# Kernel optimization log

Hardware: AMD Instinct MI355X
Metric: run time of the kernel (lower is better)

## Reference

```python
import jax, jax.numpy as jnp
import numpy as np

N = 100000   # nodes
E = 1600000  # edges
H = 256      # hidden_channels
C_IN = 1
C_OUT = 6
B = 64       # graphs in batch


def setup_inputs() -> dict:
    key = jax.random.key(0)
    ks = jax.random.split(key, 14)
    x = jax.random.normal(ks[0], (N, C_IN), jnp.float32)
    edge_index = jax.random.randint(ks[1], (2, E), 0, N, dtype=jnp.int64)
    batch = jnp.sort(jax.random.randint(ks[2], (N,), 0, B, dtype=jnp.int64))
    svm_pred = jax.random.uniform(ks[3], (B,), jnp.float32)

    def w(k, shape, fan_in):
        return jax.random.normal(k, shape, jnp.float32) * (1.0 / np.sqrt(fan_in))

    return {
        "x": x, "edge_index": edge_index, "batch": batch, "svm_pred": svm_pred,
        "W1": w(ks[4], (C_IN, H), C_IN),  "b1": jnp.zeros((H,), jnp.float32),
        "W2": w(ks[5], (H, H), H),        "b2": jnp.zeros((H,), jnp.float32),
        "W3": w(ks[6], (H, H), H),        "b3": jnp.zeros((H,), jnp.float32),
        "Wf1": w(ks[7], (H + 1, 128), H + 1), "bf1": jnp.zeros((128,), jnp.float32),
        "Wf2": w(ks[8], (128, C_OUT), 128),   "bf2": jnp.zeros((C_OUT,), jnp.float32),
    }


def reference(x, edge_index, batch, svm_pred,
              W1, b1, W2, b2, W3, b3, Wf1, bf1, Wf2, bf2):
    # --- GCN normalization (PyG GCNConv default: add self-loops, sym norm) ---
    loops = jnp.arange(N, dtype=edge_index.dtype)
    src = jnp.concatenate([edge_index[0], loops])  # [E+N]
    dst = jnp.concatenate([edge_index[1], loops])  # [E+N]
    deg = jax.ops.segment_sum(jnp.ones_like(dst, dtype=x.dtype), dst, num_segments=N)
    dinv = deg ** -0.5  # deg >= 1 due to self-loops
    norm = dinv[src] * dinv[dst]  # [E+N]

    def gcn(h, W, b):
        hw = h @ W                                   # [N, H]
        msg = hw[src] * norm[:, None]                # gather + scale
        return jax.ops.segment_sum(msg, dst, num_segments=N) + b

    # Dropout is identity in eval mode.
    h = jax.nn.relu(gcn(x, W1, b1))
    h = jax.nn.relu(gcn(h, W2, b2))
    h = jax.nn.relu(gcn(h, W3, b3))

    # global_mean_pool over graph ids
    sums = jax.ops.segment_sum(h, batch, num_segments=B)            # [B, H]
    cnts = jax.ops.segment_sum(jnp.ones((N,), h.dtype), batch, num_segments=B)
    pooled = sums / jnp.maximum(cnts, 1.0)[:, None]

    feat = jnp.concatenate([pooled, svm_pred.reshape(-1, 1).astype(h.dtype)], axis=1)
    out = jax.nn.relu(feat @ Wf1 + bf1) @ Wf2 + bf2                 # [B, 6]
    return out
```

## Files before the change

kernel.cpp:

```cpp
#include <hip/hip_runtime.h>
#include <math.h>

#define N_NODES 100000
#define N_EDGES 1600000
#define HDIM    256
#define NGRAPH  64

#define SCAN_BLK 1024
#define SCAN_NB  ((N_NODES + SCAN_BLK - 1) / SCAN_BLK)

#define FB 64

typedef __attribute__((ext_vector_type(8))) short bf16x8;
typedef __attribute__((ext_vector_type(4))) float f32x4;
typedef __attribute__((ext_vector_type(8))) unsigned short u16x8;

__device__ __forceinline__ ushort f2b(float f) {
    union { float f; unsigned u; } x; x.f = f;
    unsigned u = x.u;
    unsigned r = u + 0x7fffu + ((u >> 16) & 1u);
    return (ushort)(r >> 16);
}
__device__ __forceinline__ float b2f(ushort h) {
    union { unsigned u; float f; } x; x.u = ((unsigned)h) << 16;
    return x.f;
}

__global__ void k_count(const int* __restrict__ ei, int* __restrict__ cnt,
                        int* __restrict__ slot) {
    int t = blockIdx.x * blockDim.x + threadIdx.x;
    int e0 = t * 8;
    if (e0 >= N_EDGES) return;
    int d[8];
#pragma unroll
    for (int j = 0; j < 8; ++j) d[j] = ei[N_EDGES + e0 + j];
    int s[8];
#pragma unroll
    for (int j = 0; j < 8; ++j) s[j] = atomicAdd(&cnt[d[j]], 1);
#pragma unroll
    for (int j = 0; j < 8; ++j) slot[e0 + j] = s[j];
}

__global__ __launch_bounds__(1024) void k_scan1(const int* __restrict__ cnt,
                                                int* __restrict__ rowptr,
                                                int* __restrict__ bsum) {
    __shared__ int lds[SCAN_BLK];
    int t = threadIdx.x;
    int i = blockIdx.x * SCAN_BLK + t;
    int v = (i < N_NODES) ? cnt[i] : 0;
    lds[t] = v;
    __syncthreads();
    for (int off = 1; off < SCAN_BLK; off <<= 1) {
        int u = (t >= off) ? lds[t - off] : 0;
        __syncthreads();
        lds[t] += u;
        __syncthreads();
    }
    if (i < N_NODES) rowptr[i] = lds[t] - v;
    if (t == SCAN_BLK - 1) bsum[blockIdx.x] = lds[t];
}

__global__ __launch_bounds__(128) void k_scan2(int* __restrict__ bsum) {
    __shared__ int lds[128];
    int t = threadIdx.x;
    int v = (t < SCAN_NB) ? bsum[t] : 0;
    lds[t] = v;
    __syncthreads();
    for (int off = 1; off < 128; off <<= 1) {
        int u = (t >= off) ? lds[t - off] : 0;
        __syncthreads();
        lds[t] += u;
        __syncthreads();
    }
    if (t < SCAN_NB) bsum[t] = lds[t] - v;
}

__global__ void k_dinv_fix(const int* __restrict__ cnt, const float* __restrict__ x,
                           const int* __restrict__ bsum,
                           float* __restrict__ dinv, float* __restrict__ xd,
                           int* __restrict__ rowptr) {
    int i = blockIdx.x * blockDim.x + threadIdx.x;
    if (i < N_NODES) {
        rowptr[i] += bsum[i >> 10];
        float d = (float)(cnt[i] + 1);
        float dv = 1.0f / sqrtf(d);
        dinv[i] = dv;
        xd[i] = x[i] * dv;
        if (i == 0) rowptr[N_NODES] = N_EDGES;
    }
}

__global__ void k_fill(const int* __restrict__ ei, const int* __restrict__ rowptr,
                       const int* __restrict__ slot, int* __restrict__ colv) {
    int t = blockIdx.x * blockDim.x + threadIdx.x;
    int e0 = t * 4;
    if (e0 >= N_EDGES) return;
    int d[4], sl[4], sr[4];
#pragma unroll
    for (int j = 0; j < 4; ++j) {
        d[j] = ei[N_EDGES + e0 + j];
        sl[j] = slot[e0 + j];
        sr[j] = ei[e0 + j];
    }
    int rp[4];
#pragma unroll
    for (int j = 0; j < 4; ++j) rp[j] = rowptr[d[j]];
#pragma unroll
    for (int j = 0; j < 4; ++j) colv[rp[j] + sl[j]] = sr[j];
}

__global__ __launch_bounds__(256) void k_s(const int* __restrict__ rowptr,
                                           const int* __restrict__ colv,
                                           const float* __restrict__ xd,
                                           const float* __restrict__ dinv,
                                           float2* __restrict__ sd) {
    int wid = threadIdx.x >> 6, lane = threadIdx.x & 63;
    int node = blockIdx.x * 4 + wid;
    if (node >= N_NODES) return;
    int s = rowptr[node], e = rowptr[node + 1];
    float acc = 0.f;
    for (int idx = s + lane; idx < e; idx += 64) acc += xd[colv[idx]];
#pragma unroll
    for (int off = 32; off; off >>= 1) acc += __shfl_xor(acc, off);
    if (lane == 0) {
        float dv = dinv[node];
        sd[node] = make_float2(dv * (acc + xd[node]), dv);
    }
}

__global__ __launch_bounds__(256) void k_aggM(const int* __restrict__ rowptr,
                                              const int* __restrict__ colv,
                                              const float2* __restrict__ sd,
                                              const float* __restrict__ W1,
                                              const float* __restrict__ b1,
                                              ushort* __restrict__ M) {
    int wid = threadIdx.x >> 6, lane = threadIdx.x & 63;
    int node = blockIdx.x * 4 + wid;
    if (node >= N_NODES) return;
    int c4 = lane * 4;
    float4 w = *(const float4*)&W1[c4];
    float4 b = *(const float4*)&b1[c4];
    float2 self = sd[node];
    float a0 = self.y * fmaxf(fmaf(self.x, w.x, b.x), 0.f);
    float a1 = self.y * fmaxf(fmaf(self.x, w.y, b.y), 0.f);
    float a2 = self.y * fmaxf(fmaf(self.x, w.z, b.z), 0.f);
    float a3 = self.y * fmaxf(fmaf(self.x, w.w, b.w), 0.f);
    int s = rowptr[node], e = rowptr[node + 1];
    for (int base = s; base < e; base += 64) {
        int idx = base + lane;
        float2 p = make_float2(0.f, 0.f);
        if (idx < e) p = sd[colv[idx]];
        int rem = min(64, e - base);
        int k = 0;
        for (; k + 4 <= rem; k += 4) {
            float ps0 = __shfl(p.x, k),     pd0 = __shfl(p.y, k);
            float ps1 = __shfl(p.x, k + 1), pd1 = __shfl(p.y, k + 1);
            float ps2 = __shfl(p.x, k + 2), pd2 = __shfl(p.y, k + 2);
            float ps3 = __shfl(p.x, k + 3), pd3 = __shfl(p.y, k + 3);
            a0 += pd0 * fmaxf(fmaf(ps0, w.x, b.x), 0.f)
                + pd1 * fmaxf(fmaf(ps1, w.x, b.x), 0.f)
                + pd2 * fmaxf(fmaf(ps2, w.x, b.x), 0.f)
                + pd3 * fmaxf(fmaf(ps3, w.x, b.x), 0.f);
            a1 += pd0 * fmaxf(fmaf(ps0, w.y, b.y), 0.f)
                + pd1 * fmaxf(fmaf(ps1, w.y, b.y), 0.f)
                + pd2 * fmaxf(fmaf(ps2, w.y, b.y), 0.f)
                + pd3 * fmaxf(fmaf(ps3, w.y, b.y), 0.f);
            a2 += pd0 * fmaxf(fmaf(ps0, w.z, b.z), 0.f)
                + pd1 * fmaxf(fmaf(ps1, w.z, b.z), 0.f)
                + pd2 * fmaxf(fmaf(ps2, w.z, b.z), 0.f)
                + pd3 * fmaxf(fmaf(ps3, w.z, b.z), 0.f);
            a3 += pd0 * fmaxf(fmaf(ps0, w.w, b.w), 0.f)
                + pd1 * fmaxf(fmaf(ps1, w.w, b.w), 0.f)
                + pd2 * fmaxf(fmaf(ps2, w.w, b.w), 0.f)
                + pd3 * fmaxf(fmaf(ps3, w.w, b.w), 0.f);
        }
        for (; k < rem; ++k) {
            float ps = __shfl(p.x, k);
            float pd = __shfl(p.y, k);
            a0 += pd * fmaxf(fmaf(ps, w.x, b.x), 0.f);
            a1 += pd * fmaxf(fmaf(ps, w.y, b.y), 0.f);
            a2 += pd * fmaxf(fmaf(ps, w.z, b.z), 0.f);
            a3 += pd * fmaxf(fmaf(ps, w.w, b.w), 0.f);
        }
    }
    float dvi = self.y;
    ushort4 o;
    o.x = f2b(a0 * dvi);
    o.y = f2b(a1 * dvi);
    o.z = f2b(a2 * dvi);
    o.w = f2b(a3 * dvi);
    *(ushort4*)&M[(size_t)node * HDIM + c4] = o;
}

__global__ __launch_bounds__(256) void k_packW2(const float* __restrict__ Wa,
                                                ushort* __restrict__ Wpa,
                                                const float* __restrict__ Wb,
                                                ushort* __restrict__ Wpb) {
    int bid = blockIdx.x;
    const float* W = (bid < 32) ? Wa : Wb;
    ushort* Wp = (bid < 32) ? Wpa : Wpb;
    int t = (bid & 31) * 256 + threadIdx.x;
    int lane = t & 63;
    int nt = (t >> 6) & 15;
    int k0 = t >> 10;
    int col = nt * 16 + (lane & 15);
    int kb = k0 * 32 + (lane >> 4) * 8;
    ushort o[8];
#pragma unroll
    for (int j = 0; j < 8; ++j) o[j] = f2b(W[(size_t)(kb + j) * HDIM + col]);
    *(ushort4*)&Wp[(size_t)t * 8 + 0] = make_ushort4(o[0], o[1], o[2], o[3]);
    *(ushort4*)&Wp[(size_t)t * 8 + 4] = make_ushort4(o[4], o[5], o[6], o[7]);
}

__global__ __launch_bounds__(256) void k_g23(
    const ushort* __restrict__ M,
    const ushort* __restrict__ Wp2, const float* __restrict__ b2,
    const ushort* __restrict__ Wp3, const float* __restrict__ dinv,
    ushort* __restrict__ C) {
    __shared__ __align__(16) ushort lds[FB * 256];
    char* ldsb = (char*)lds;
    int tid = threadIdx.x;
    int wave = tid >> 6, lane = tid & 63;
    int l = wave * 16 + (lane & 15);
    int node = blockIdx.x * FB + l;
    int kgrp = lane >> 4;
    bool ok = node < N_NODES;
    unsigned swz = ((unsigned)(l & 7)) << 4;
    unsigned rowb = (unsigned)l * 512;

    f32x4 acc[16];
#pragma unroll
    for (int nt = 0; nt < 16; ++nt) acc[nt] = (f32x4){0.f, 0.f, 0.f, 0.f};
    const ushort* ap = M + (size_t)(ok ? node : 0) * HDIM + kgrp * 8;
#pragma unroll 1
    for (int k0 = 0; k0 < 8; ++k0) {
        bf16x8 bf = *(const bf16x8*)(ap + k0 * 32);
        if (!ok) bf = (bf16x8){0, 0, 0, 0, 0, 0, 0, 0};
        const ushort* wp = Wp2 + ((size_t)k0 * 1024 + lane) * 8;
#pragma unroll
        for (int nt = 0; nt < 16; ++nt) {
            bf16x8 a = *(const bf16x8*)(wp + (size_t)nt * 512);
            acc[nt] = __builtin_amdgcn_mfma_f32_16x16x32_bf16(a, bf, acc[nt], 0, 0, 0);
        }
    }

#pragma unroll
    for (int nt = 0; nt < 16; ++nt) {
        int f = nt * 16 + kgrp * 4;
        float4 bv = *(const float4*)&b2[f];
        uint2 pk;
        pk.x = (unsigned)f2b(fmaxf(acc[nt][0] + bv.x, 0.f)) |
               ((unsigned)f2b(fmaxf(acc[nt][1] + bv.y, 0.f)) << 16);
        pk.y = (unsigned)f2b(fmaxf(acc[nt][2] + bv.z, 0.f)) |
               ((unsigned)f2b(fmaxf(acc[nt][3] + bv.w, 0.f)) << 16);
        *(uint2*)(ldsb + rowb + (((unsigned)(f * 2)) ^ swz)) = pk;
    }
    __syncthreads();

#pragma unroll
    for (int nt = 0; nt < 16; ++nt) acc[nt] = (f32x4){0.f, 0.f, 0.f, 0.f};
#pragma unroll 1
    for (int k0 = 0; k0 < 8; ++k0) {
        bf16x8 bf = *(const bf16x8*)(ldsb + rowb + (((unsigned)(16 * kgrp + 64 * k0)) ^ swz));
        const ushort* wp = Wp3 + ((size_t)k0 * 1024 + lane) * 8;
#pragma unroll
        for (int nt = 0; nt < 16; ++nt) {
            bf16x8 a = *(const bf16x8*)(wp + (size_t)nt * 512);
            acc[nt] = __builtin_amdgcn_mfma_f32_16x16x32_bf16(a, bf, acc[nt], 0, 0, 0);
        }
    }
    if (ok) {
        float dv = dinv[node];
        size_t base = (size_t)node * HDIM + kgrp * 4;
#pragma unroll
        for (int nt = 0; nt < 16; ++nt) {
            ushort4 o;
            o.x = f2b(acc[nt][0] * dv);
            o.y = f2b(acc[nt][1] * dv);
            o.z = f2b(acc[nt][2] * dv);
            o.w = f2b(acc[nt][3] * dv);
            *(ushort4*)&C[base + nt * 16] = o;
        }
    }
}

__global__ __launch_bounds__(256) void k_agg(const ushort* __restrict__ g,
                                             const int* __restrict__ rowptr,
                                             const int* __restrict__ colv,
                                             const float* __restrict__ dinv,
                                             const float* __restrict__ bias,
                                             ushort* __restrict__ hout) {
    int wid = threadIdx.x >> 6, lane = threadIdx.x & 63;
    int node = blockIdx.x * 4 + wid;
    if (node >= N_NODES) return;
    int half = lane >> 5;
    int l32 = lane & 31;
    int c8 = l32 * 8;
    float acc[8];
    if (half == 0) {
        u16x8 v = *(const u16x8*)&g[(size_t)node * HDIM + c8];
#pragma unroll
        for (int j = 0; j < 8; ++j) acc[j] = b2f(v[j]);
    } else {
#pragma unroll
        for (int j = 0; j < 8; ++j) acc[j] = 0.f;
    }
    int s = rowptr[node], e = rowptr[node + 1];
    int i = s;
    for (; i + 8 <= e; i += 8) {
        int base = i + half * 4;
        int n0 = colv[base + 0];
        int n1 = colv[base + 1];
        int n2 = colv[base + 2];
        int n3 = colv[base + 3];
        u16x8 v0 = *(const u16x8*)&g[(size_t)n0 * HDIM + c8];
        u16x8 v1 = *(const u16x8*)&g[(size_t)n1 * HDIM + c8];
        u16x8 v2 = *(const u16x8*)&g[(size_t)n2 * HDIM + c8];
        u16x8 v3 = *(const u16x8*)&g[(size_t)n3 * HDIM + c8];
#pragma unroll
        for (int j = 0; j < 8; ++j)
            acc[j] += (b2f(v0[j]) + b2f(v1[j])) + (b2f(v2[j]) + b2f(v3[j]));
    }
    if (i + 4 <= e) {
        int base = i + half * 2;
        int n0 = colv[base + 0];
        int n1 = colv[base + 1];
        u16x8 v0 = *(const u16x8*)&g[(size_t)n0 * HDIM + c8];
        u16x8 v1 = *(const u16x8*)&g[(size_t)n1 * HDIM + c8];
#pragma unroll
        for (int j = 0; j < 8; ++j) acc[j] += b2f(v0[j]) + b2f(v1[j]);
        i += 4;
    }
    if (i + 2 <= e) {
        int n = colv[i + half];
        u16x8 v = *(const u16x8*)&g[(size_t)n * HDIM + c8];
#pragma unroll
        for (int j = 0; j < 8; ++j) acc[j] += b2f(v[j]);
        i += 2;
    }
    if (i < e && half == 0) {
        int n = colv[i];
        u16x8 v = *(const u16x8*)&g[(size_t)n * HDIM + c8];
#pragma unroll
        for (int j = 0; j < 8; ++j) acc[j] += b2f(v[j]);
    }
#pragma unroll
    for (int j = 0; j < 8; ++j) acc[j] += __shfl_xor(acc[j], 32);
    if (half == 0) {
        float dv = dinv[node];
        float4 bl = *(const float4*)&bias[c8];
        float4 bh = *(const float4*)&bias[c8 + 4];
        float bj[8] = {bl.x, bl.y, bl.z, bl.w, bh.x, bh.y, bh.z, bh.w};
        u16x8 ov;
#pragma unroll
        for (int j = 0; j < 8; ++j)
            ov[j] = f2b(fmaxf(fmaf(acc[j], dv, bj[j]), 0.f));
        *(u16x8*)&hout[(size_t)node * HDIM + c8] = ov;
    }
}

__global__ __launch_bounds__(128) void k_bounds(const int* __restrict__ batch,
                                                int* __restrict__ startb,
                                                float* __restrict__ pooled) {
    int t = threadIdx.x;
    if (t <= NGRAPH) {
        int lo = 0, hi = N_NODES;
        while (lo < hi) {
            int mid = (lo + hi) >> 1;
            if (batch[mid] < t) lo = mid + 1; else hi = mid;
        }
        startb[t] = lo;
    }
    for (int i = t; i < NGRAPH * HDIM; i += 128) pooled[i] = 0.f;
}

__global__ __launch_bounds__(256) void k_pool(const ushort* __restrict__ h,
                                              const int* __restrict__ startb,
                                              float* __restrict__ pooled) {
    int b = blockIdx.x >> 3, c = blockIdx.x & 7;
    int s0 = startb[b], e0 = startb[b + 1];
    int len = e0 - s0;
    if (len <= 0) return;
    int per = (len + 7) >> 3;
    int is = s0 + c * per;
    int ie = min(is + per, e0);
    if (is >= ie) return;
    int j = threadIdx.x;
    float sum = 0.f;
    for (int n = is; n < ie; ++n) sum += b2f(h[(size_t)n * HDIM + j]);
    atomicAdd(&pooled[b * HDIM + j], sum);
}

__global__ __launch_bounds__(128) void k_mlp(const float* __restrict__ pooled,
                                             const int* __restrict__ startb,
                                             const float* __restrict__ svm,
                                             const float* __restrict__ Wf1,
                                             const float* __restrict__ bf1,
                                             const float* __restrict__ Wf2,
                                             const float* __restrict__ bf2,
                                             float* __restrict__ out) {
    __shared__ float fl[257];
    __shared__ float hl[128];
    int b = blockIdx.x;
    int j = threadIdx.x;
    float cntb = fmaxf((float)(startb[b + 1] - startb[b]), 1.0f);
    for (int k = j; k < 256; k += 128) fl[k] = pooled[b * HDIM + k] / cntb;
    if (j == 0) fl[256] = svm[b];
    __syncthreads();
    float acc = bf1[j];
    for (int k = 0; k < 257; ++k) acc = fmaf(fl[k], Wf1[k * 128 + j], acc);
    hl[j] = fmaxf(acc, 0.f);
    __syncthreads();
    if (j < 6) {
        float o = bf2[j];
        for (int k = 0; k < 128; ++k) o = fmaf(hl[k], Wf2[k * 6 + j], o);
        out[b * 6 + j] = o;
    }
}

static inline size_t al256(size_t x) { return (x + 255) & ~(size_t)255; }

extern "C" void kernel_launch(void* const* d_in, const int* in_sizes, int n_in,
                              void* d_out, int out_size, void* d_ws, size_t ws_size,
                              hipStream_t stream) {
    const float* x    = (const float*)d_in[0];
    const int*   ei   = (const int*)d_in[1];
    const int*   batch= (const int*)d_in[2];
    const float* svm  = (const float*)d_in[3];
    const float* W1   = (const float*)d_in[4];
    const float* b1   = (const float*)d_in[5];
    const float* W2   = (const float*)d_in[6];
    const float* b2   = (const float*)d_in[7];
    const float* W3   = (const float*)d_in[8];
    const float* b3   = (const float*)d_in[9];
    const float* Wf1  = (const float*)d_in[10];
    const float* bf1  = (const float*)d_in[11];
    const float* Wf2  = (const float*)d_in[12];
    const float* bf2  = (const float*)d_in[13];
    float* out = (float*)d_out;

    char* w = (char*)d_ws;
    int*    cnt    = (int*)w;    w += al256((size_t)N_NODES * 4);
    int*    rowptr = (int*)w;    w += al256((size_t)(N_NODES + 1) * 4);
    int*    slot   = (int*)w;    w += al256((size_t)N_EDGES * 4);
    int*    colv   = (int*)w;    w += al256((size_t)N_EDGES * 4);
    float*  dinv   = (float*)w;  w += al256((size_t)N_NODES * 4);
    float*  xd     = (float*)w;  w += al256((size_t)N_NODES * 4);
    float2* sd     = (float2*)w; w += al256((size_t)N_NODES * 8);
    int*    startb = (int*)w;    w += al256(65 * 4);
    int*    bsum   = (int*)w;    w += al256((size_t)SCAN_NB * 4);
    float*  pooled = (float*)w;  w += al256((size_t)NGRAPH * HDIM * 4);
    ushort* Wp2    = (ushort*)w; w += al256((size_t)8 * 16 * 64 * 8 * 2);
    ushort* Wp3    = (ushort*)w; w += al256((size_t)8 * 16 * 64 * 8 * 2);
    ushort* bigA   = (ushort*)w; w += al256((size_t)N_NODES * HDIM * 2);
    ushort* bigB   = (ushort*)w; w += al256((size_t)N_NODES * HDIM * 2);

    const int nblkN = (N_NODES + 255) / 256;
    const int nblkW = (N_NODES + 3) / 4;
    const int nblkF = (N_NODES + FB - 1) / FB;

    hipMemsetAsync(cnt, 0, (size_t)N_NODES * 4, stream);
    k_count<<<(N_EDGES / 8 + 255) / 256, 256, 0, stream>>>(ei, cnt, slot);
    k_scan1<<<SCAN_NB, SCAN_BLK, 0, stream>>>(cnt, rowptr, bsum);
    k_scan2<<<1, 128, 0, stream>>>(bsum);
    k_dinv_fix<<<nblkN, 256, 0, stream>>>(cnt, x, bsum, dinv, xd, rowptr);
    k_fill<<<(N_EDGES / 4 + 255) / 256, 256, 0, stream>>>(ei, rowptr, slot, colv);

    k_packW2<<<64, 256, 0, stream>>>(W2, Wp2, W3, Wp3);

    k_s<<<nblkW, 256, 0, stream>>>(rowptr, colv, xd, dinv, sd);

    k_aggM<<<nblkW, 256, 0, stream>>>(rowptr, colv, sd, W1, b1, bigA);

    k_g23<<<nblkF, 256, 0, stream>>>(bigA, Wp2, b2, Wp3, dinv, bigB);

    k_agg<<<nblkW, 256, 0, stream>>>(bigB, rowptr, colv, dinv, b3, bigA);

    k_bounds<<<1, 128, 0, stream>>>(batch, startb, pooled);
    k_pool<<<NGRAPH * 8, 256, 0, stream>>>(bigA, startb, pooled);
    k_mlp<<<NGRAPH, 128, 0, stream>>>(pooled, startb, svm, Wf1, bf1, Wf2, bf2, out);
}
```

Baseline: 466.7 us.

## Fuse final GCN aggregation with mean pooling and widen edge-per-thread work

```diff
diff --git a/kernel.cpp b/kernel.cpp
--- a/kernel.cpp
+++ b/kernel.cpp
@@ -29,16 +29,16 @@
 __global__ void k_count(const int* __restrict__ ei, int* __restrict__ cnt,
                         int* __restrict__ slot) {
     int t = blockIdx.x * blockDim.x + threadIdx.x;
-    int e0 = t * 8;
+    int e0 = t * 16;
     if (e0 >= N_EDGES) return;
-    int d[8];
-#pragma unroll
-    for (int j = 0; j < 8; ++j) d[j] = ei[N_EDGES + e0 + j];
-    int s[8];
-#pragma unroll
-    for (int j = 0; j < 8; ++j) s[j] = atomicAdd(&cnt[d[j]], 1);
-#pragma unroll
-    for (int j = 0; j < 8; ++j) slot[e0 + j] = s[j];
+    int d[16];
+#pragma unroll
+    for (int j = 0; j < 16; ++j) d[j] = ei[N_EDGES + e0 + j];
+    int s[16];
+#pragma unroll
+    for (int j = 0; j < 16; ++j) s[j] = atomicAdd(&cnt[d[j]], 1);
+#pragma unroll
+    for (int j = 0; j < 16; ++j) slot[e0 + j] = s[j];
 }
 
 __global__ __launch_bounds__(1024) void k_scan1(const int* __restrict__ cnt,
@@ -93,20 +93,20 @@
 __global__ void k_fill(const int* __restrict__ ei, const int* __restrict__ rowptr,
                        const int* __restrict__ slot, int* __restrict__ colv) {
     int t = blockIdx.x * blockDim.x + threadIdx.x;
-    int e0 = t * 4;
+    int e0 = t * 8;
     if (e0 >= N_EDGES) return;
-    int d[4], sl[4], sr[4];
-#pragma unroll
-    for (int j = 0; j < 4; ++j) {
+    int d[8], sl[8], sr[8];
+#pragma unroll
+    for (int j = 0; j < 8; ++j) {
         d[j] = ei[N_EDGES + e0 + j];
         sl[j] = slot[e0 + j];
         sr[j] = ei[e0 + j];
     }
-    int rp[4];
-#pragma unroll
-    for (int j = 0; j < 4; ++j) rp[j] = rowptr[d[j]];
-#pragma unroll
-    for (int j = 0; j < 4; ++j) colv[rp[j] + sl[j]] = sr[j];
+    int rp[8];
+#pragma unroll
+    for (int j = 0; j < 8; ++j) rp[j] = rowptr[d[j]];
+#pragma unroll
+    for (int j = 0; j < 8; ++j) colv[rp[j] + sl[j]] = sr[j];
 }
 
 __global__ __launch_bounds__(256) void k_s(const int* __restrict__ rowptr,
@@ -284,28 +284,30 @@
     }
 }
 
-__global__ __launch_bounds__(256) void k_agg(const ushort* __restrict__ g,
-                                             const int* __restrict__ rowptr,
-                                             const int* __restrict__ colv,
-                                             const float* __restrict__ dinv,
-                                             const float* __restrict__ bias,
-                                             ushort* __restrict__ hout) {
+__global__ __launch_bounds__(1024) void k_agg_pool(
+    const ushort* __restrict__ g, const int* __restrict__ rowptr,
+    const int* __restrict__ colv, const float* __restrict__ dinv,
+    const float* __restrict__ bias, const int* __restrict__ batch,
+    float* __restrict__ pooled) {
+    __shared__ float srow[16][256];
+    __shared__ int wbid[16];
     int wid = threadIdx.x >> 6, lane = threadIdx.x & 63;
-    int node = blockIdx.x * 4 + wid;
-    if (node >= N_NODES) return;
+    int node = blockIdx.x * 16 + wid;
+    bool ok = node < N_NODES;
+    int nd = ok ? node : N_NODES - 1;
     int half = lane >> 5;
     int l32 = lane & 31;
     int c8 = l32 * 8;
     float acc[8];
     if (half == 0) {
-        u16x8 v = *(const u16x8*)&g[(size_t)node * HDIM + c8];
+        u16x8 v = *(const u16x8*)&g[(size_t)nd * HDIM + c8];
 #pragma unroll
         for (int j = 0; j < 8; ++j) acc[j] = b2f(v[j]);
     } else {
 #pragma unroll
         for (int j = 0; j < 8; ++j) acc[j] = 0.f;
     }
-    int s = rowptr[node], e = rowptr[node + 1];
+    int s = rowptr[nd], e = rowptr[nd + 1];
     int i = s;
     for (; i + 8 <= e; i += 8) {
         int base = i + half * 4;
@@ -347,15 +349,32 @@
 #pragma unroll
     for (int j = 0; j < 8; ++j) acc[j] += __shfl_xor(acc[j], 32);
     if (half == 0) {
-        float dv = dinv[node];
+        float dv = dinv[nd];
         float4 bl = *(const float4*)&bias[c8];
         float4 bh = *(const float4*)&bias[c8 + 4];
         float bj[8] = {bl.x, bl.y, bl.z, bl.w, bh.x, bh.y, bh.z, bh.w};
-        u16x8 ov;
-#pragma unroll
-        for (int j = 0; j < 8; ++j)
-            ov[j] = f2b(fmaxf(fmaf(acc[j], dv, bj[j]), 0.f));
-        *(u16x8*)&hout[(size_t)node * HDIM + c8] = ov;
+#pragma unroll
+        for (int j = 0; j < 8; ++j) {
+            float v = fmaxf(fmaf(acc[j], dv, bj[j]), 0.f);
+            srow[wid][c8 + j] = ok ? v : 0.f;
+        }
+        if (l32 == 0) wbid[wid] = batch[nd];
+    }
+    __syncthreads();
+    if (threadIdx.x < 256) {
+        int j = threadIdx.x;
+        float run = srow[0][j];
+        int cur = wbid[0];
+        for (int w = 1; w < 16; ++w) {
+            int b = wbid[w];
+            if (b != cur) {
+                atomicAdd(&pooled[cur * HDIM + j], run);
+                run = 0.f;
+                cur = b;
+            }
+            run += srow[w][j];
+        }
+        atomicAdd(&pooled[cur * HDIM + j], run);
     }
 }
 
@@ -372,23 +391,6 @@
         startb[t] = lo;
     }
     for (int i = t; i < NGRAPH * HDIM; i += 128) pooled[i] = 0.f;
-}
-
-__global__ __launch_bounds__(256) void k_pool(const ushort* __restrict__ h,
-                                              const int* __restrict__ startb,
-                                              float* __restrict__ pooled) {
-    int b = blockIdx.x >> 3, c = blockIdx.x & 7;
-    int s0 = startb[b], e0 = startb[b + 1];
-    int len = e0 - s0;
-    if (len <= 0) return;
-    int per = (len + 7) >> 3;
-    int is = s0 + c * per;
-    int ie = min(is + per, e0);
-    if (is >= ie) return;
-    int j = threadIdx.x;
-    float sum = 0.f;
-    for (int n = is; n < ie; ++n) sum += b2f(h[(size_t)n * HDIM + j]);
-    atomicAdd(&pooled[b * HDIM + j], sum);
 }
 
 __global__ __launch_bounds__(128) void k_mlp(const float* __restrict__ pooled,
@@ -458,13 +460,14 @@
     const int nblkN = (N_NODES + 255) / 256;
     const int nblkW = (N_NODES + 3) / 4;
     const int nblkF = (N_NODES + FB - 1) / FB;
+    const int nblkP = (N_NODES + 15) / 16;
 
     hipMemsetAsync(cnt, 0, (size_t)N_NODES * 4, stream);
-    k_count<<<(N_EDGES / 8 + 255) / 256, 256, 0, stream>>>(ei, cnt, slot);
+    k_count<<<(N_EDGES / 16 + 255) / 256, 256, 0, stream>>>(ei, cnt, slot);
     k_scan1<<<SCAN_NB, SCAN_BLK, 0, stream>>>(cnt, rowptr, bsum);
     k_scan2<<<1, 128, 0, stream>>>(bsum);
     k_dinv_fix<<<nblkN, 256, 0, stream>>>(cnt, x, bsum, dinv, xd, rowptr);
-    k_fill<<<(N_EDGES / 4 + 255) / 256, 256, 0, stream>>>(ei, rowptr, slot, colv);
+    k_fill<<<(N_EDGES / 8 + 255) / 256, 256, 0, stream>>>(ei, rowptr, slot, colv);
 
     k_packW2<<<64, 256, 0, stream>>>(W2, Wp2, W3, Wp3);
 
@@ -474,9 +477,9 @@
 
     k_g23<<<nblkF, 256, 0, stream>>>(bigA, Wp2, b2, Wp3, dinv, bigB);
 
-    k_agg<<<nblkW, 256, 0, stream>>>(bigB, rowptr, colv, dinv, b3, bigA);
-
     k_bounds<<<1, 128, 0, stream>>>(batch, startb, pooled);
-    k_pool<<<NGRAPH * 8, 256, 0, stream>>>(bigA, startb, pooled);
+
+    k_agg_pool<<<nblkP, 1024, 0, stream>>>(bigB, rowptr, colv, dinv, b3, batch, pooled);
+
     k_mlp<<<NGRAPH, 128, 0, stream>>>(pooled, startb, svm, Wf1, bf1, Wf2, bf2, out);
 }
```

After: 413.7 us. 11.3% less time.
